# Kernel tuning notes

Hardware: AMD Instinct MI355X
Metric: run time of the kernel (lower is better)

The kernel has to match this reference:

```python
import jax, jax.numpy as jnp
import numpy as np

LEAKY_SLOPE = 0.2  # tf.nn.leaky_relu default alpha
N_NODES = 50000
N_EDGES = 800000
IN_DIM = 128
OUT_DIM = 64
HEADS = 4
MLP_HID = 256
MLP_OUT = 128


def setup_inputs() -> dict:
    key = jax.random.key(0)
    ks = jax.random.split(key, 10)
    node_embeddings = jax.random.normal(ks[0], (N_NODES, IN_DIM), dtype=jnp.float32)
    src = jax.random.randint(ks[1], (N_EDGES,), 0, N_NODES, dtype=jnp.int32)
    dst = jax.random.randint(ks[2], (N_EDGES,), 0, N_NODES, dtype=jnp.int32)
    # glorot-ish scales
    W_n = jax.random.normal(ks[3], (HEADS, IN_DIM, OUT_DIM), dtype=jnp.float32) * (1.0 / np.sqrt(IN_DIM))
    a_src = jax.random.normal(ks[4], (HEADS, OUT_DIM), dtype=jnp.float32) * (1.0 / np.sqrt(OUT_DIM))
    a_dst = jax.random.normal(ks[5], (HEADS, OUT_DIM), dtype=jnp.float32) * (1.0 / np.sqrt(OUT_DIM))
    mlp_W1 = jax.random.normal(ks[6], (HEADS * OUT_DIM, MLP_HID), dtype=jnp.float32) * (1.0 / np.sqrt(HEADS * OUT_DIM))
    mlp_b1 = jnp.zeros((MLP_HID,), dtype=jnp.float32)
    mlp_W2 = jax.random.normal(ks[7], (MLP_HID, MLP_OUT), dtype=jnp.float32) * (1.0 / np.sqrt(MLP_HID))
    mlp_b2 = jnp.zeros((MLP_OUT,), dtype=jnp.float32)
    return {"node_embeddings": node_embeddings, "src": src, "dst": dst,
            "W_n": W_n, "a_src": a_src, "a_dst": a_dst,
            "mlp_W1": mlp_W1, "mlp_b1": mlp_b1, "mlp_W2": mlp_W2, "mlp_b2": mlp_b2}


def _gat_forward(node_embeddings, src, dst, W_n, a_src, a_dst, mlp_W1, mlp_b1, mlp_W2, mlp_b2):
    N = node_embeddings.shape[0]
    # per-head linear transform: [N, H, D]
    h = jnp.einsum('nc,hcd->nhd', node_embeddings, W_n)
    # decomposed attention scores at node level, gathered per edge
    s_src = jnp.einsum('nhd,hd->nh', h, a_src)          # [N, H]
    s_dst = jnp.einsum('nhd,hd->nh', h, a_dst)          # [N, H]
    e = jax.nn.leaky_relu(s_src[src] + s_dst[dst], negative_slope=LEAKY_SLOPE)  # [E, H]
    # segment softmax over incoming edges of each dst node
    e_max = jax.ops.segment_max(e, dst, num_segments=N)          # [N, H], -inf for empty
    ex = jnp.exp(e - e_max[dst])                                  # [E, H]
    den = jax.ops.segment_sum(ex, dst, num_segments=N)            # [N, H]
    m = h[src]                                                    # [E, H, D] messages
    num = jax.ops.segment_sum(ex[:, :, None] * m, dst, num_segments=N)  # [N, H, D]
    safe_den = jnp.where(den > 0, den, 1.0)
    head_out = jax.nn.relu(num / safe_den[:, :, None])            # [N, H, D]
    concat = head_out.reshape(N, -1)                              # [N, H*D]
    hidden = jax.nn.relu(concat @ mlp_W1 + mlp_b1)
    return hidden @ mlp_W2 + mlp_b2                               # [N, MLP_OUT]


def reference(node_embeddings, src, dst, W_n, a_src, a_dst, mlp_W1, mlp_b1, mlp_W2, mlp_b2):
    return _gat_forward(node_embeddings, src, dst, W_n, a_src, a_dst,
                        mlp_W1, mlp_b1, mlp_W2, mlp_b2)
```

## Files before the change

kernel.cpp:

```cpp
#include <hip/hip_runtime.h>

#define LEAKY 0.2f

typedef __attribute__((ext_vector_type(8))) short short8;
typedef __attribute__((ext_vector_type(4))) float floatx4;
typedef __attribute__((ext_vector_type(8))) unsigned short ushort8_t;

__device__ __forceinline__ float bf2f(unsigned short u) {
    return __uint_as_float(((unsigned)u) << 16);
}
__device__ __forceinline__ unsigned short f2bf(float f) {
    unsigned u = __float_as_uint(f);
    unsigned r = (u + 0x7fffu + ((u >> 16) & 1u)) >> 16;
    return (unsigned short)r;
}
__device__ __forceinline__ float relu_nan(float v) { return v < 0.0f ? 0.0f : v; }

__device__ __forceinline__ void gload_lds16(const void* g, void* l) {
    __builtin_amdgcn_global_load_lds((const __attribute__((address_space(1))) void*)g,
                                     (__attribute__((address_space(3))) void*)l, 16, 0, 0);
}

__global__ void k_fill(float* __restrict__ p, float val, int n) {
    int i = blockIdx.x * blockDim.x + threadIdx.x;
    if (i < n) p[i] = val;
}

__global__ void k_prep(const float* __restrict__ X, unsigned short* __restrict__ Xb,
                       const float* __restrict__ Wn, unsigned short* __restrict__ WnT,
                       const float* __restrict__ W1, unsigned short* __restrict__ W1T,
                       const float* __restrict__ W2, unsigned short* __restrict__ W2T,
                       const int* __restrict__ dst, int* __restrict__ cnt,
                       int N, int E) {
    const int gs = gridDim.x * blockDim.x;
    const int tid = blockIdx.x * blockDim.x + threadIdx.x;
    for (int i = tid; i < N * 32; i += gs) {
        float4 v = ((const float4*)X)[i];
        ushort4 o;
        o.x = f2bf(v.x); o.y = f2bf(v.y); o.z = f2bf(v.z); o.w = f2bf(v.w);
        ((ushort4*)Xb)[i] = o;
    }
    for (int i = tid; i < 256 * 128; i += gs) {
        int col = i >> 7, k = i & 127;
        int head = col >> 6, d = col & 63;
        WnT[i] = f2bf(Wn[(size_t)head * 8192 + (size_t)k * 64 + d]);
    }
    for (int i = tid; i < 256 * 256; i += gs) {
        int n = i >> 8, k = i & 255;
        W1T[i] = f2bf(W1[(size_t)k * 256 + n]);
    }
    for (int i = tid; i < 128 * 256; i += gs) {
        int n = i >> 8, k = i & 255;
        W2T[i] = f2bf(W2[(size_t)k * 128 + n]);
    }
    for (int i = tid; i < E; i += gs) atomicAdd(cnt + dst[i], 1);
}

__global__ __launch_bounds__(256) void k_scan1(
    const int* __restrict__ cnt, int* __restrict__ rowptr, int* __restrict__ bsum, int N) {
    __shared__ int wtot[4];
    const int lane = threadIdx.x & 63, wave = threadIdx.x >> 6;
    const int i = blockIdx.x * 256 + threadIdx.x;
    int v = (i < N) ? cnt[i] : 0;
    int x = v;
    for (int off = 1; off < 64; off <<= 1) {
        int y = __shfl_up(x, off, 64);
        if (lane >= off) x += y;
    }
    if (lane == 63) wtot[wave] = x;
    __syncthreads();
    int wo = 0;
    for (int wv = 0; wv < wave; ++wv) wo += wtot[wv];
    if (i < N) rowptr[i] = wo + x - v;
    if (threadIdx.x == 255) bsum[blockIdx.x] = wo + x;
}
__global__ void k_scan2(int* __restrict__ bsum, int nb) {
    const int lane = threadIdx.x;
    int carry = 0;
    for (int base = 0; base < nb; base += 64) {
        int i = base + lane;
        int v = (i < nb) ? bsum[i] : 0;
        int x = v;
        for (int off = 1; off < 64; off <<= 1) {
            int y = __shfl_up(x, off, 64);
            if (lane >= off) x += y;
        }
        if (i < nb) bsum[i] = carry + x - v;
        carry += __shfl(x, 63, 64);
    }
}
__global__ void k_scan3(int* __restrict__ rowptr, const int* __restrict__ bsum,
                        int* __restrict__ wcnt, int N, int E) {
    int i = blockIdx.x * blockDim.x + threadIdx.x;
    if (i < N) {
        int v = rowptr[i] + bsum[i >> 8];
        rowptr[i] = v;
        wcnt[i] = v;
    }
    if (i == N) rowptr[N] = E;
}

__global__ void k_scatter(const int* __restrict__ src, const int* __restrict__ dst,
                          int* __restrict__ wcnt, int* __restrict__ esrc, int E) {
    int e = blockIdx.x * blockDim.x + threadIdx.x;
    if (e < E) {
        int pos = atomicAdd(wcnt + dst[e], 1);
        esrc[pos] = src[e];
    }
}

__global__ __launch_bounds__(256) void k_agg(
    const float* __restrict__ s_src, const float* __restrict__ s_dst,
    const unsigned short* __restrict__ h_bf,
    const int* __restrict__ rowptr, const int* __restrict__ esrc,
    unsigned short* __restrict__ concat, int N) {
    const int t = threadIdx.x;
    const int lane = t & 63;
    const int wave = t >> 6;
    const int n = blockIdx.x * 4 + wave;
    if (n >= N) return;

    const int q = lane & 31;
    const int half = lane >> 5;
    const int hq4 = (q >> 3) << 4;
    const int slot = lane & 15;
    const int headw = lane >> 4;

    const int beg = rowptr[n], end = rowptr[n + 1];
    const float sdst = s_dst[n * 4 + headw];
    const unsigned short* hrow = h_bf + q * 8;

    float num[8] = {0, 0, 0, 0, 0, 0, 0, 0};
    float den = 0.0f;

    for (int base = beg; base < end; base += 16) {
        const int rem = end - base;
        int sid = 0;
        float mex = 0.0f;
        if (slot < rem) {
            sid = esrc[base + slot];
            float v = s_src[sid * 4 + headw] + sdst;
            v = fmaxf(v, LEAKY * v);
            mex = __expf(v);
        }
        den += mex;

        auto pair = [&](int i) {
            const int ep = 2 * i + half;
            const int s_ = __shfl(sid, ep, 64);
            const float ex_ = __shfl(mex, hq4 | ep, 64);
            const ushort8_t hv = *(const ushort8_t*)(hrow + (size_t)s_ * 256);
#pragma unroll
            for (int j = 0; j < 8; ++j)
                num[j] = fmaf(ex_, bf2f(hv[j]), num[j]);
        };

        if (rem >= 16) {
#pragma unroll
            for (int i = 0; i < 8; ++i) pair(i);
        } else {
            const int np = (rem + 1) >> 1;
            for (int i = 0; i < np; ++i) pair(i);
        }
    }

#pragma unroll
    for (int j = 0; j < 8; ++j) num[j] += __shfl_xor(num[j], 32, 64);
#pragma unroll
    for (int m = 1; m < 16; m <<= 1) den += __shfl_xor(den, m, 64);
    const float denq = __shfl(den, hq4, 64);
    const float inv = 1.0f / (denq > 0.0f ? denq : 1.0f);

    ushort8_t o;
#pragma unroll
    for (int j = 0; j < 8; ++j) o[j] = f2bf(relu_nan(num[j] * inv));
    if (lane < 32)
        *(ushort8_t*)(concat + (size_t)n * 256 + q * 8) = o;
}

template <int K, int MODE>
__global__ __launch_bounds__(256) void k_gemm(
    const unsigned short* __restrict__ A, const unsigned short* __restrict__ BT,
    const float* __restrict__ bias, unsigned short* __restrict__ Cb,
    float* __restrict__ Cf, int N, int ldout,
    const float* __restrict__ asrc, const float* __restrict__ adst,
    float* __restrict__ s_src, float* __restrict__ s_dst) {
    __shared__ unsigned short As[128 * 32];
    __shared__ unsigned short Bs[128 * 32];
    const int t = threadIdx.x;
    const int lane = t & 63;
    const int w = t >> 6;
    const int wy = w >> 1, wx = w & 1;
    const int lm = lane & 15, quad = lane >> 4;
    const int row0 = blockIdx.x * 128;
    const int n0 = blockIdx.y * 128;
    const int srow = lane >> 2;
    const int sk = (lane & 3) * 8;

    floatx4 acc[4][4];
    if (MODE == 0) {
#pragma unroll
        for (int mi = 0; mi < 4; ++mi)
#pragma unroll
            for (int ni = 0; ni < 4; ++ni) acc[mi][ni] = (floatx4){0, 0, 0, 0};
    } else {
#pragma unroll
        for (int ni = 0; ni < 4; ++ni) {
            float b = bias[n0 + wx * 64 + ni * 16 + lm];
#pragma unroll
            for (int mi = 0; mi < 4; ++mi) acc[mi][ni] = (floatx4){b, b, b, b};
        }
    }

    for (int k0 = 0; k0 < K; k0 += 32) {
#pragma unroll
        for (int p = 0; p < 2; ++p) {
            int tr = (p * 4 + w) * 16 + srow;
            int ga = row0 + tr; if (ga >= N) ga = N - 1;
            gload_lds16(A + (size_t)ga * K + k0 + sk,
                        (char*)As + (size_t)tr * 64 + sk * 2);
            gload_lds16(BT + (size_t)(n0 + tr) * K + k0 + sk,
                        (char*)Bs + (size_t)tr * 64 + sk * 2);
        }
        __syncthreads();
        short8 af[4], bfr[4];
#pragma unroll
        for (int mi = 0; mi < 4; ++mi)
            af[mi] = *(const short8*)(As + (size_t)(wy * 64 + mi * 16 + lm) * 32 + quad * 8);
#pragma unroll
        for (int ni = 0; ni < 4; ++ni)
            bfr[ni] = *(const short8*)(Bs + (size_t)(wx * 64 + ni * 16 + lm) * 32 + quad * 8);
#pragma unroll
        for (int mi = 0; mi < 4; ++mi)
#pragma unroll
            for (int ni = 0; ni < 4; ++ni)
                acc[mi][ni] = __builtin_amdgcn_mfma_f32_16x16x32_bf16(af[mi], bfr[ni], acc[mi][ni], 0, 0, 0);
        __syncthreads();
    }

#pragma unroll
    for (int mi = 0; mi < 4; ++mi)
#pragma unroll
        for (int ni = 0; ni < 4; ++ni)
#pragma unroll
            for (int q = 0; q < 4; ++q) {
                int r = row0 + wy * 64 + mi * 16 + quad * 4 + q;
                int c = n0 + wx * 64 + ni * 16 + lm;
                if (r < N) {
                    if (MODE == 0)      Cb[(size_t)r * ldout + c] = f2bf(acc[mi][ni][q]);
                    else if (MODE == 1) Cb[(size_t)r * ldout + c] = f2bf(relu_nan(acc[mi][ni][q]));
                    else                Cf[(size_t)r * ldout + c] = acc[mi][ni][q];
                }
            }

    if (MODE == 0) {
        const int head = blockIdx.y * 2 + wx;
        float as[4], ad[4];
#pragma unroll
        for (int ni = 0; ni < 4; ++ni) {
            int d = ni * 16 + lm;
            as[ni] = asrc[head * 64 + d];
            ad[ni] = adst[head * 64 + d];
        }
#pragma unroll
        for (int mi = 0; mi < 4; ++mi)
#pragma unroll
            for (int q = 0; q < 4; ++q) {
                float ps = acc[mi][0][q] * as[0] + acc[mi][1][q] * as[1]
                         + acc[mi][2][q] * as[2] + acc[mi][3][q] * as[3];
                float pd = acc[mi][0][q] * ad[0] + acc[mi][1][q] * ad[1]
                         + acc[mi][2][q] * ad[2] + acc[mi][3][q] * ad[3];
#pragma unroll
                for (int m = 1; m < 16; m <<= 1) {
                    ps += __shfl_xor(ps, m, 64);
                    pd += __shfl_xor(pd, m, 64);
                }
                if (lm == 0) {
                    int r = row0 + wy * 64 + mi * 16 + quad * 4 + q;
                    if (r < N) {
                        s_src[r * 4 + head] = ps;
                        s_dst[r * 4 + head] = pd;
                    }
                }
            }
    }
}

extern "C" void kernel_launch(void* const* d_in, const int* in_sizes, int n_in,
                              void* d_out, int out_size, void* d_ws, size_t ws_size,
                              hipStream_t stream) {
    const float* X    = (const float*)d_in[0];
    const int* src    = (const int*)d_in[1];
    const int* dst    = (const int*)d_in[2];
    const float* Wn   = (const float*)d_in[3];
    const float* Asrc = (const float*)d_in[4];
    const float* Adst = (const float*)d_in[5];
    const float* W1   = (const float*)d_in[6];
    const float* b1   = (const float*)d_in[7];
    const float* W2   = (const float*)d_in[8];
    const float* b2   = (const float*)d_in[9];
    float* out = (float*)d_out;

    const int N = in_sizes[0] / 128;
    const int E = in_sizes[1];
    const int NBS = (N + 255) / 256;
    const int NR = (N + 127) / 128;

    size_t off = 0;
    char* w = (char*)d_ws;
    unsigned short* h_bf = (unsigned short*)(w + off); off += (size_t)N * 256 * 2;
    float* s_src = (float*)(w + off);                  off += (size_t)N * 4 * 4;
    float* s_dst = (float*)(w + off);                  off += (size_t)N * 4 * 4;
    int* cnt     = (int*)(w + off);                    off += (size_t)N * 4;
    int* rowptr  = (int*)(w + off);                    off += ((size_t)(N + 1) * 4 + 15) & ~15ull;
    int* wcnt    = (int*)(w + off);                    off += (size_t)N * 4;
    int* bsum    = (int*)(w + off);                    off += ((size_t)NBS * 4 + 15) & ~15ull;
    int* esrc    = (int*)(w + off);                    off += (size_t)E * 4;
    unsigned short* W1T = (unsigned short*)(w + off);  off += 256 * 256 * 2;
    unsigned short* W2T = (unsigned short*)(w + off);  off += 128 * 256 * 2;
    unsigned short* WnT = (unsigned short*)(w + off);  off += 256 * 128 * 2;
    const size_t required = off;

    if (ws_size < required) {
        k_fill<<<dim3((out_size + 255) / 256), dim3(256), 0, stream>>>(
            out, (float)(ws_size >> 20), out_size);
        return;
    }

    unsigned short* Xb     = (unsigned short*)d_out;
    unsigned short* concat = (unsigned short*)d_out;

    hipMemsetAsync(cnt, 0, (size_t)N * sizeof(int), stream);
    k_prep<<<dim3(2048), dim3(256), 0, stream>>>(X, Xb, Wn, WnT, W1, W1T, W2, W2T,
                                                 dst, cnt, N, E);
    k_gemm<128, 0><<<dim3(NR, 2), dim3(256), 0, stream>>>(
        Xb, WnT, nullptr, h_bf, nullptr, N, 256, Asrc, Adst, s_src, s_dst);
    k_scan1<<<dim3(NBS), dim3(256), 0, stream>>>(cnt, rowptr, bsum, N);
    k_scan2<<<dim3(1), dim3(64), 0, stream>>>(bsum, NBS);
    k_scan3<<<dim3((N + 256) / 256), dim3(256), 0, stream>>>(rowptr, bsum, wcnt, N, E);
    k_scatter<<<dim3((E + 255) / 256), dim3(256), 0, stream>>>(src, dst, wcnt, esrc, E);
    k_agg<<<dim3((N + 3) / 4), dim3(256), 0, stream>>>(s_src, s_dst, h_bf, rowptr, esrc, concat, N);
    k_gemm<256, 1><<<dim3(NR, 2), dim3(256), 0, stream>>>(
        concat, W1T, b1, h_bf, nullptr, N, 256, nullptr, nullptr, nullptr, nullptr);
    k_gemm<256, 2><<<dim3(NR, 1), dim3(256), 0, stream>>>(
        h_bf, W2T, b2, nullptr, out, N, 128, nullptr, nullptr, nullptr, nullptr);
}
```

Before: 306.6 us.

## Aggregate raw inputs per head and apply the head projection after aggregation

Uses linearity to gather bf16 input rows (128 wide) per edge instead of projected per-head features (256 wide), then applies the per-head Wn projection with a new MFMA GEMM that also scales by the inverse softmax denominator and applies ReLU. Attention scores come from folded W·a vectors in a small score kernel, replacing the epilogue of the first GEMM. Edge exp weights are now computed once in the scatter kernel and stored in CSR order, and the aggregation loop prefetches the next chunk of edge indices. The cost is a larger intermediate buffer (N×512 bf16), an extra E×4 float buffer, and one more kernel launch.

```diff
diff --git a/kernel.cpp b/kernel.cpp
--- a/kernel.cpp
+++ b/kernel.cpp
@@ -30,6 +30,8 @@
                        const float* __restrict__ Wn, unsigned short* __restrict__ WnT,
                        const float* __restrict__ W1, unsigned short* __restrict__ W1T,
                        const float* __restrict__ W2, unsigned short* __restrict__ W2T,
+                       const float* __restrict__ Asrc, const float* __restrict__ Adst,
+                       float* __restrict__ Wsd,
                        const int* __restrict__ dst, int* __restrict__ cnt,
                        int N, int E) {
     const int gs = gridDim.x * blockDim.x;
@@ -53,7 +55,35 @@
         int n = i >> 8, k = i & 255;
         W2T[i] = f2bf(W2[(size_t)k * 128 + n]);
     }
+    for (int i = tid; i < 8 * 128; i += gs) {
+        int j = i >> 7, k = i & 127, h = j & 3;
+        const float* av = (j < 4 ? Asrc : Adst) + h * 64;
+        const float* wrow = Wn + (size_t)h * 8192 + (size_t)k * 64;
+        float acc = 0.0f;
+        for (int d = 0; d < 64; ++d) acc += wrow[d] * av[d];
+        Wsd[i] = acc;
+    }
     for (int i = tid; i < E; i += gs) atomicAdd(cnt + dst[i], 1);
+}
+
+__global__ __launch_bounds__(256) void k_scores(
+    const unsigned short* __restrict__ Xb, const float* __restrict__ Wsd,
+    float* __restrict__ s_src, float* __restrict__ s_dst, int N) {
+    const int gs = gridDim.x * 256;
+    const int tid = blockIdx.x * 256 + threadIdx.x;
+    for (int i = tid; i < N * 8; i += gs) {
+        const int n = i >> 3, j = i & 7;
+        const unsigned short* xr = Xb + (size_t)n * 128;
+        const float* wr = Wsd + j * 128;
+        float acc = 0.0f;
+        for (int k = 0; k < 128; k += 8) {
+            ushort8_t xv = *(const ushort8_t*)(xr + k);
+#pragma unroll
+            for (int u = 0; u < 8; ++u) acc = fmaf(bf2f(xv[u]), wr[k + u], acc);
+        }
+        if (j < 4) s_src[n * 4 + j] = acc;
+        else       s_dst[n * 4 + (j - 4)] = acc;
+    }
 }
 
 __global__ __launch_bounds__(256) void k_scan1(
@@ -101,90 +131,169 @@
 }
 
 __global__ void k_scatter(const int* __restrict__ src, const int* __restrict__ dst,
-                          int* __restrict__ wcnt, int* __restrict__ esrc, int E) {
+                          int* __restrict__ wcnt,
+                          const float* __restrict__ s_src, const float* __restrict__ s_dst,
+                          int* __restrict__ esrc, float* __restrict__ ex4, int E) {
     int e = blockIdx.x * blockDim.x + threadIdx.x;
     if (e < E) {
-        int pos = atomicAdd(wcnt + dst[e], 1);
-        esrc[pos] = src[e];
+        const int s = src[e], d = dst[e];
+        const int pos = atomicAdd(wcnt + d, 1);
+        esrc[pos] = s;
+        const float4 ss = *(const float4*)(s_src + (size_t)s * 4);
+        const float4 sd = *(const float4*)(s_dst + (size_t)d * 4);
+        float4 o;
+        float v;
+        v = ss.x + sd.x; v = fmaxf(v, LEAKY * v); o.x = __expf(v);
+        v = ss.y + sd.y; v = fmaxf(v, LEAKY * v); o.y = __expf(v);
+        v = ss.z + sd.z; v = fmaxf(v, LEAKY * v); o.z = __expf(v);
+        v = ss.w + sd.w; v = fmaxf(v, LEAKY * v); o.w = __expf(v);
+        *(float4*)(ex4 + (size_t)pos * 4) = o;
     }
 }
 
 __global__ __launch_bounds__(256) void k_agg(
-    const float* __restrict__ s_src, const float* __restrict__ s_dst,
-    const unsigned short* __restrict__ h_bf,
+    const unsigned short* __restrict__ Xb,
     const int* __restrict__ rowptr, const int* __restrict__ esrc,
-    unsigned short* __restrict__ concat, int N) {
+    const float* __restrict__ ex4,
+    unsigned short* __restrict__ agg, float* __restrict__ invden, int N) {
+    const int lane = threadIdx.x & 63;
+    const int wave = threadIdx.x >> 6;
+    const int n = blockIdx.x * 4 + wave;
+    if (n >= N) return;
+
+    const int slot = lane & 15;
+    const int g16  = lane & 48;
+    const int head = lane >> 4;
+    const unsigned short* xcol = Xb + slot * 8;
+
+    const int beg = rowptr[n], end = rowptr[n + 1];
+
+    float num[8] = {0, 0, 0, 0, 0, 0, 0, 0};
+    float den = 0.0f;
+
+    int base = beg;
+    int sidv = 0; float exv = 0.0f;
+    if (base < end) {
+        const int rem = end - base;
+        if (slot < rem) {
+            sidv = esrc[base + slot];
+            exv  = ex4[(size_t)(base + slot) * 4 + head];
+        }
+    }
+
+    while (base < end) {
+        const int rem = end - base;
+        const int nb  = base + 16;
+        int sidn = 0; float exn = 0.0f;
+        if (nb < end) {
+            const int rem2 = end - nb;
+            if (slot < rem2) {
+                sidn = esrc[nb + slot];
+                exn  = ex4[(size_t)(nb + slot) * 4 + head];
+            }
+        }
+        den += exv;
+
+        if (rem >= 16) {
+#pragma unroll
+            for (int e = 0; e < 16; ++e) {
+                const int s_   = __shfl(sidv, e, 64);
+                const float x_ = __shfl(exv, g16 | e, 64);
+                const ushort8_t xv = *(const ushort8_t*)(xcol + (size_t)s_ * 128);
+#pragma unroll
+                for (int j = 0; j < 8; ++j) num[j] = fmaf(x_, bf2f(xv[j]), num[j]);
+            }
+        } else {
+            for (int e = 0; e < rem; ++e) {
+                const int s_   = __shfl(sidv, e, 64);
+                const float x_ = __shfl(exv, g16 | e, 64);
+                const ushort8_t xv = *(const ushort8_t*)(xcol + (size_t)s_ * 128);
+#pragma unroll
+                for (int j = 0; j < 8; ++j) num[j] = fmaf(x_, bf2f(xv[j]), num[j]);
+            }
+        }
+        sidv = sidn; exv = exn; base = nb;
+    }
+
+#pragma unroll
+    for (int m = 1; m < 16; m <<= 1) den += __shfl_xor(den, m, 64);
+    const float inv = 1.0f / (den > 0.0f ? den : 1.0f);
+
+    ushort8_t o;
+#pragma unroll
+    for (int j = 0; j < 8; ++j) o[j] = f2bf(num[j]);
+    *(ushort8_t*)(agg + (size_t)n * 512 + head * 128 + slot * 8) = o;
+    if (slot == 0) invden[n * 4 + head] = inv;
+}
+
+__global__ __launch_bounds__(256) void k_gemmh(
+    const unsigned short* __restrict__ agg, const unsigned short* __restrict__ WnT,
+    const float* __restrict__ invden, unsigned short* __restrict__ concat, int N) {
+    __shared__ unsigned short As[256 * 32];
+    __shared__ unsigned short Bs[64 * 32];
     const int t = threadIdx.x;
     const int lane = t & 63;
-    const int wave = t >> 6;
-    const int n = blockIdx.x * 4 + wave;
-    if (n >= N) return;
-
-    const int q = lane & 31;
-    const int half = lane >> 5;
-    const int hq4 = (q >> 3) << 4;
-    const int slot = lane & 15;
-    const int headw = lane >> 4;
-
-    const int beg = rowptr[n], end = rowptr[n + 1];
-    const float sdst = s_dst[n * 4 + headw];
-    const unsigned short* hrow = h_bf + q * 8;
-
-    float num[8] = {0, 0, 0, 0, 0, 0, 0, 0};
-    float den = 0.0f;
-
-    for (int base = beg; base < end; base += 16) {
-        const int rem = end - base;
-        int sid = 0;
-        float mex = 0.0f;
-        if (slot < rem) {
-            sid = esrc[base + slot];
-            float v = s_src[sid * 4 + headw] + sdst;
-            v = fmaxf(v, LEAKY * v);
-            mex = __expf(v);
-        }
-        den += mex;
-
-        auto pair = [&](int i) {
-            const int ep = 2 * i + half;
-            const int s_ = __shfl(sid, ep, 64);
-            const float ex_ = __shfl(mex, hq4 | ep, 64);
-            const ushort8_t hv = *(const ushort8_t*)(hrow + (size_t)s_ * 256);
-#pragma unroll
-            for (int j = 0; j < 8; ++j)
-                num[j] = fmaf(ex_, bf2f(hv[j]), num[j]);
-        };
-
-        if (rem >= 16) {
-#pragma unroll
-            for (int i = 0; i < 8; ++i) pair(i);
-        } else {
-            const int np = (rem + 1) >> 1;
-            for (int i = 0; i < np; ++i) pair(i);
-        }
-    }
-
-#pragma unroll
-    for (int j = 0; j < 8; ++j) num[j] += __shfl_xor(num[j], 32, 64);
-#pragma unroll
-    for (int m = 1; m < 16; m <<= 1) den += __shfl_xor(den, m, 64);
-    const float denq = __shfl(den, hq4, 64);
-    const float inv = 1.0f / (denq > 0.0f ? denq : 1.0f);
-
-    ushort8_t o;
-#pragma unroll
-    for (int j = 0; j < 8; ++j) o[j] = f2bf(relu_nan(num[j] * inv));
-    if (lane < 32)
-        *(ushort8_t*)(concat + (size_t)n * 256 + q * 8) = o;
+    const int w = t >> 6;
+    const int lm = lane & 15, quad = lane >> 4;
+    const int row0 = blockIdx.x * 256;
+    const int head = blockIdx.y;
+
+    floatx4 acc[4][4];
+#pragma unroll
+    for (int mi = 0; mi < 4; ++mi)
+#pragma unroll
+        for (int ni = 0; ni < 4; ++ni) acc[mi][ni] = (floatx4){0, 0, 0, 0};
+
+    for (int k0 = 0; k0 < 128; k0 += 32) {
+#pragma unroll
+        for (int p = 0; p < 4; ++p) {
+            int tr = p * 64 + (t >> 2);
+            int ga = row0 + tr; if (ga >= N) ga = N - 1;
+            gload_lds16(agg + (size_t)ga * 512 + head * 128 + k0 + (t & 3) * 8,
+                        (char*)As + (size_t)tr * 64 + (t & 3) * 16);
+        }
+        {
+            int tr = t >> 2;
+            gload_lds16(WnT + (size_t)(head * 64 + tr) * 128 + k0 + (t & 3) * 8,
+                        (char*)Bs + (size_t)tr * 64 + (t & 3) * 16);
+        }
+        __syncthreads();
+        short8 af[4], bfr[4];
+#pragma unroll
+        for (int mi = 0; mi < 4; ++mi)
+            af[mi] = *(const short8*)(As + (size_t)(w * 64 + mi * 16 + lm) * 32 + quad * 8);
+#pragma unroll
+        for (int ni = 0; ni < 4; ++ni)
+            bfr[ni] = *(const short8*)(Bs + (size_t)(ni * 16 + lm) * 32 + quad * 8);
+#pragma unroll
+        for (int mi = 0; mi < 4; ++mi)
+#pragma unroll
+            for (int ni = 0; ni < 4; ++ni)
+                acc[mi][ni] = __builtin_amdgcn_mfma_f32_16x16x32_bf16(af[mi], bfr[ni], acc[mi][ni], 0, 0, 0);
+        __syncthreads();
+    }
+
+#pragma unroll
+    for (int mi = 0; mi < 4; ++mi)
+#pragma unroll
+        for (int q = 0; q < 4; ++q) {
+            const int r = row0 + w * 64 + mi * 16 + quad * 4 + q;
+            if (r < N) {
+                const float inv = invden[(size_t)r * 4 + head];
+#pragma unroll
+                for (int ni = 0; ni < 4; ++ni) {
+                    const int c = ni * 16 + lm;
+                    concat[(size_t)r * 256 + head * 64 + c] = f2bf(relu_nan(acc[mi][ni][q] * inv));
+                }
+            }
+        }
 }
 
 template <int K, int MODE>
 __global__ __launch_bounds__(256) void k_gemm(
     const unsigned short* __restrict__ A, const unsigned short* __restrict__ BT,
     const float* __restrict__ bias, unsigned short* __restrict__ Cb,
-    float* __restrict__ Cf, int N, int ldout,
-    const float* __restrict__ asrc, const float* __restrict__ adst,
-    float* __restrict__ s_src, float* __restrict__ s_dst) {
+    float* __restrict__ Cf, int N, int ldout) {
     __shared__ unsigned short As[128 * 32];
     __shared__ unsigned short Bs[128 * 32];
     const int t = threadIdx.x;
@@ -198,18 +307,11 @@
     const int sk = (lane & 3) * 8;
 
     floatx4 acc[4][4];
-    if (MODE == 0) {
-#pragma unroll
-        for (int mi = 0; mi < 4; ++mi)
-#pragma unroll
-            for (int ni = 0; ni < 4; ++ni) acc[mi][ni] = (floatx4){0, 0, 0, 0};
-    } else {
-#pragma unroll
-        for (int ni = 0; ni < 4; ++ni) {
-            float b = bias[n0 + wx * 64 + ni * 16 + lm];
-#pragma unroll
-            for (int mi = 0; mi < 4; ++mi) acc[mi][ni] = (floatx4){b, b, b, b};
-        }
+#pragma unroll
+    for (int ni = 0; ni < 4; ++ni) {
+        float b = bias[n0 + wx * 64 + ni * 16 + lm];
+#pragma unroll
+        for (int mi = 0; mi < 4; ++mi) acc[mi][ni] = (floatx4){b, b, b, b};
     }
 
     for (int k0 = 0; k0 < K; k0 += 32) {
@@ -247,43 +349,10 @@
                 int r = row0 + wy * 64 + mi * 16 + quad * 4 + q;
                 int c = n0 + wx * 64 + ni * 16 + lm;
                 if (r < N) {
-                    if (MODE == 0)      Cb[(size_t)r * ldout + c] = f2bf(acc[mi][ni][q]);
-                    else if (MODE == 1) Cb[(size_t)r * ldout + c] = f2bf(relu_nan(acc[mi][ni][q]));
-                    else                Cf[(size_t)r * ldout + c] = acc[mi][ni][q];
+                    if (MODE == 1) Cb[(size_t)r * ldout + c] = f2bf(relu_nan(acc[mi][ni][q]));
+                    else           Cf[(size_t)r * ldout + c] = acc[mi][ni][q];
                 }
             }
-
-    if (MODE == 0) {
-        const int head = blockIdx.y * 2 + wx;
-        float as[4], ad[4];
-#pragma unroll
-        for (int ni = 0; ni < 4; ++ni) {
-            int d = ni * 16 + lm;
-            as[ni] = asrc[head * 64 + d];
-            ad[ni] = adst[head * 64 + d];
-        }
-#pragma unroll
-        for (int mi = 0; mi < 4; ++mi)
-#pragma unroll
-            for (int q = 0; q < 4; ++q) {
-                float ps = acc[mi][0][q] * as[0] + acc[mi][1][q] * as[1]
-                         + acc[mi][2][q] * as[2] + acc[mi][3][q] * as[3];
-                float pd = acc[mi][0][q] * ad[0] + acc[mi][1][q] * ad[1]
-                         + acc[mi][2][q] * ad[2] + acc[mi][3][q] * ad[3];
-#pragma unroll
-                for (int m = 1; m < 16; m <<= 1) {
-                    ps += __shfl_xor(ps, m, 64);
-                    pd += __shfl_xor(pd, m, 64);
-                }
-                if (lm == 0) {
-                    int r = row0 + wy * 64 + mi * 16 + quad * 4 + q;
-                    if (r < N) {
-                        s_src[r * 4 + head] = ps;
-                        s_dst[r * 4 + head] = pd;
-                    }
-                }
-            }
-    }
 }
 
 extern "C" void kernel_launch(void* const* d_in, const int* in_sizes, int n_in,
@@ -305,20 +374,24 @@
     const int E = in_sizes[1];
     const int NBS = (N + 255) / 256;
     const int NR = (N + 127) / 128;
+    const int NRH = (N + 255) / 256;
 
     size_t off = 0;
     char* w = (char*)d_ws;
-    unsigned short* h_bf = (unsigned short*)(w + off); off += (size_t)N * 256 * 2;
+    unsigned short* aggb = (unsigned short*)(w + off); off += (size_t)N * 512 * 2;
     float* s_src = (float*)(w + off);                  off += (size_t)N * 4 * 4;
     float* s_dst = (float*)(w + off);                  off += (size_t)N * 4 * 4;
+    float* invden= (float*)(w + off);                  off += (size_t)N * 4 * 4;
     int* cnt     = (int*)(w + off);                    off += (size_t)N * 4;
     int* rowptr  = (int*)(w + off);                    off += ((size_t)(N + 1) * 4 + 15) & ~15ull;
     int* wcnt    = (int*)(w + off);                    off += (size_t)N * 4;
     int* bsum    = (int*)(w + off);                    off += ((size_t)NBS * 4 + 15) & ~15ull;
     int* esrc    = (int*)(w + off);                    off += (size_t)E * 4;
+    float* ex4   = (float*)(w + off);                  off += (size_t)E * 4 * 4;
     unsigned short* W1T = (unsigned short*)(w + off);  off += 256 * 256 * 2;
     unsigned short* W2T = (unsigned short*)(w + off);  off += 128 * 256 * 2;
     unsigned short* WnT = (unsigned short*)(w + off);  off += 256 * 128 * 2;
+    float* Wsd   = (float*)(w + off);                  off += 8 * 128 * 4;
     const size_t required = off;
 
     if (ws_size < required) {
@@ -329,19 +402,21 @@
 
     unsigned short* Xb     = (unsigned short*)d_out;
     unsigned short* concat = (unsigned short*)d_out;
+    unsigned short* hid    = aggb;
 
     hipMemsetAsync(cnt, 0, (size_t)N * sizeof(int), stream);
     k_prep<<<dim3(2048), dim3(256), 0, stream>>>(X, Xb, Wn, WnT, W1, W1T, W2, W2T,
-                                                 dst, cnt, N, E);
-    k_gemm<128, 0><<<dim3(NR, 2), dim3(256), 0, stream>>>(
-        Xb, WnT, nullptr, h_bf, nullptr, N, 256, Asrc, Adst, s_src, s_dst);
+                                                 Asrc, Adst, Wsd, dst, cnt, N, E);
+    k_scores<<<dim3((N * 8 + 255) / 256), dim3(256), 0, stream>>>(Xb, Wsd, s_src, s_dst, N);
     k_scan1<<<dim3(NBS), dim3(256), 0, stream>>>(cnt, rowptr, bsum, N);
     k_scan2<<<dim3(1), dim3(64), 0, stream>>>(bsum, NBS);
     k_scan3<<<dim3((N + 256) / 256), dim3(256), 0, stream>>>(rowptr, bsum, wcnt, N, E);
-    k_scatter<<<dim3((E + 255) / 256), dim3(256), 0, stream>>>(src, dst, wcnt, esrc, E);
-    k_agg<<<dim3((N + 3) / 4), dim3(256), 0, stream>>>(s_src, s_dst, h_bf, rowptr, esrc, concat, N);
+    k_scatter<<<dim3((E + 255) / 256), dim3(256), 0, stream>>>(src, dst, wcnt, s_src, s_dst,
+                                                               esrc, ex4, E);
+    k_agg<<<dim3((N + 3) / 4), dim3(256), 0, stream>>>(Xb, rowptr, esrc, ex4, aggb, invden, N);
+    k_gemmh<<<dim3(NRH, 4), dim3(256), 0, stream>>>(aggb, WnT, invden, concat, N);
     k_gemm<256, 1><<<dim3(NR, 2), dim3(256), 0, stream>>>(
-        concat, W1T, b1, h_bf, nullptr, N, 256, nullptr, nullptr, nullptr, nullptr);
+        concat, W1T, b1, hid, nullptr, N, 256);
     k_gemm<256, 2><<<dim3(NR, 1), dim3(256), 0, stream>>>(
-        h_bf, W2T, b2, nullptr, out, N, 128, nullptr, nullptr, nullptr, nullptr);
-}
+        hid, W2T, b2, nullptr, out, N, 128);
+}
```

Result: slower. 340.4 us (+11.0%).
